# Optimization experiments

Hardware: AMD Instinct MI355X
Metric: run time of the kernel (lower is better)

Reference implementation:

```python
import jax, jax.numpy as jnp
import numpy as np

H = 16          # num_heads
NB = 32         # pos_bias_num_buckets
EPS = 1e-8      # RMSNorm eps


def setup_inputs() -> dict:
    key = jax.random.key(0)
    ks = jax.random.split(key, 8)
    B, L, K, R, M, Dm, Dq = 2, 32, 2, 64, 128, 2048, 2048
    x = jax.random.normal(ks[0], (B, L, K, R, Dm), jnp.float32)
    past_ca_hidden_states = jax.random.normal(ks[1], (B, L, M, Dm), jnp.float32)
    past_ca_attention_mask = jax.random.bernoulli(ks[2], 0.95, (B, L, M)).astype(jnp.float32)
    ln_scale = jnp.ones((Dm,), jnp.float32)
    q_w = jax.random.normal(ks[3], (Dq, Dm), jnp.float32) * 0.02      # torch Linear weight [out,in]
    kv_w = jax.random.normal(ks[4], (2 * Dq, Dm), jnp.float32) * 0.02
    out_w = jax.random.normal(ks[5], (Dm, Dq), jnp.float32) * 0.02
    bias_table = jax.random.normal(ks[6], (NB, H), jnp.float32) * 0.02  # relative_attention_bias.weight
    return dict(x=x, past_ca_hidden_states=past_ca_hidden_states,
                past_ca_attention_mask=past_ca_attention_mask,
                ln_scale=ln_scale, q_w=q_w, kv_w=kv_w, out_w=out_w,
                bias_table=bias_table)


def _rel_bias(bias_table, r, m):
    # linear bucketing, bidirectional=True (RelativePositionBias._relative_position_bucket_linear)
    mn = -(NB // 2) - (NB % 2 - 1)   # -15 for NB=32
    mx = NB // 2                      # 16
    rel = jnp.arange(m)[None, :] - jnp.arange(r)[:, None]   # memory - query, [r, m]
    buckets = jnp.clip(rel, mn, mx) - mn                    # in [0, NB)
    return jnp.transpose(bias_table[buckets], (2, 0, 1))    # [H, r, m]


def reference(x, past_ca_hidden_states, past_ca_attention_mask,
              ln_scale, q_w, kv_w, out_w, bias_table):
    B, L, K, R, Dm = x.shape
    M = past_ca_hidden_states.shape[2]
    Dq = q_w.shape[0]
    dh = Dq // H

    # RMSNorm (p=-1: full norm)
    rms = jnp.linalg.norm(x, axis=-1, keepdims=True) * (Dm ** -0.5)
    xn = (x / (rms + EPS)) * ln_scale

    # projections (no bias)
    q = jnp.einsum('blkrc,qc->blkrq', xn, q_w)                 # [B,L,K,R,Dq]
    kv = jnp.einsum('blmc,qc->blmq', past_ca_hidden_states, kv_w)  # [B,L,M,2Dq]
    k = kv[..., :Dq]
    v = kv[..., Dq:]

    # split heads
    q = q.reshape(B, L, K, R, H, dh).transpose(0, 1, 2, 4, 3, 5)  # [B,L,K,H,R,dh]
    k = k.reshape(B, L, M, H, dh).transpose(0, 1, 3, 2, 4)        # [B,L,H,M,dh]
    v = v.reshape(B, L, M, H, dh).transpose(0, 1, 3, 2, 4)        # [B,L,H,M,dh]

    # NOTE: original applies NO 1/sqrt(dh) scaling
    scores = jnp.einsum('blkhrd,blhmd->blkhrm', q, k)             # [B,L,K,H,R,M]
    scores = scores + _rel_bias(bias_table, R, M)                 # broadcast [H,R,M]
    mask_add = (1.0 - past_ca_attention_mask) * -10000.0          # [B,L,M]
    scores = scores + mask_add[:, :, None, None, None, :]

    attn = jax.nn.softmax(scores, axis=-1)
    out = jnp.einsum('blkhrm,blhmd->blkhrd', attn, v)             # [B,L,K,H,R,dh]
    out = out.transpose(0, 1, 2, 4, 3, 5).reshape(B, L, K, R, Dq)  # merge heads '(h d)'
    out = jnp.einsum('blkrq,cq->blkrc', out, out_w)                # final_proj
    return out + x, attn
```

## Files before the change

### kernel.cpp

```cpp
#include <hip/hip_runtime.h>

typedef _Float16 f16;
typedef _Float16 f16x8 __attribute__((ext_vector_type(8)));
typedef float f32x4 __attribute__((ext_vector_type(4)));

#define LDS_GL16(g, l) __builtin_amdgcn_global_load_lds( \
    (const __attribute__((address_space(1))) void*)(g),  \
    (__attribute__((address_space(3))) void*)(l), 16, 0, 0)
#define VMCNT(N) asm volatile("s_waitcnt vmcnt(" #N ")" ::: "memory")
#define BAR() __builtin_amdgcn_s_barrier()

__global__ __launch_bounds__(256) void conv4_kern(
        const float* __restrict__ s0, f16* __restrict__ d0,
        const float* __restrict__ s1, f16* __restrict__ d1,
        const float* __restrict__ s2, f16* __restrict__ d2,
        const float* __restrict__ s3, f16* __restrict__ d3) {
    int b = blockIdx.x;
    const float* in; f16* out; long base;
    if (b < 2048)       { in = s0; out = d0; base = (long)b * 2048; }
    else if (b < 6144)  { in = s1; out = d1; base = (long)(b - 2048) * 2048; }
    else if (b < 8192)  { in = s2; out = d2; base = (long)(b - 6144) * 2048; }
    else                { in = s3; out = d3; base = (long)(b - 8192) * 2048; }
    long o = base + threadIdx.x * 8;
    float4 a = *(const float4*)(in + o);
    float4 c = *(const float4*)(in + o + 4);
    f16x8 v = { (f16)a.x,(f16)a.y,(f16)a.z,(f16)a.w,
                (f16)c.x,(f16)c.y,(f16)c.z,(f16)c.w };
    *(f16x8*)(out + o) = v;
}

__global__ __launch_bounds__(256) void rmsnorm_kern(const float* __restrict__ x,
                                                    const float* __restrict__ scale,
                                                    f16* __restrict__ out) {
    long base = (long)blockIdx.x * 2048 + threadIdx.x * 8;
    float4 a = *(const float4*)(x + base);
    float4 b = *(const float4*)(x + base + 4);
    float ss = a.x*a.x + a.y*a.y + a.z*a.z + a.w*a.w
             + b.x*b.x + b.y*b.y + b.z*b.z + b.w*b.w;
    #pragma unroll
    for (int d = 1; d < 64; d <<= 1) ss += __shfl_xor(ss, d, 64);
    __shared__ float red[4];
    if ((threadIdx.x & 63) == 0) red[threadIdx.x >> 6] = ss;
    __syncthreads();
    ss = red[0] + red[1] + red[2] + red[3];
    float inv = 1.0f / (sqrtf(ss * (1.0f / 2048.0f)) + 1e-8f);
    int c = threadIdx.x * 8;
    float4 s1 = *(const float4*)(scale + c);
    float4 s2 = *(const float4*)(scale + c + 4);
    f16x8 v = { (f16)(a.x*inv*s1.x),(f16)(a.y*inv*s1.y),(f16)(a.z*inv*s1.z),(f16)(a.w*inv*s1.w),
                (f16)(b.x*inv*s2.x),(f16)(b.y*inv*s2.y),(f16)(b.z*inv*s2.z),(f16)(b.w*inv*s2.w) };
    *(f16x8*)(out + base) = v;
}

template<int EPI>
__device__ __forceinline__ void gemm256_body(
        const f16* __restrict__ A, const f16* __restrict__ B,
        f16* __restrict__ Ch, float* __restrict__ Cf,
        const float* __restrict__ resid, int N, int Kd, int m0, int n0) {
    alignas(16) __shared__ f16 lds[65536];
    int tid = threadIdx.x, lane = tid & 63;
    int wid = tid >> 6, wm = wid >> 2, wn = wid & 3;
    int lr = lane & 15, g = lane >> 4;
    int iL = tid >> 3, cb = tid & 7;

    long goff[8]; int doff[8];
    #pragma unroll
    for (int rd = 0; rd < 2; ++rd) {
        int rA0 = iL + rd * 128;
        goff[0 + rd] = (long)(m0 + rA0) * Kd + ((cb ^ (rA0 & 7)) << 3);
        doff[0 + rd] = rA0 * 64 + cb * 8;
        int rB0 = (iL & 31) + ((iL >> 5) + rd * 2) * 64;
        goff[2 + rd] = (long)(n0 + rB0) * Kd + ((cb ^ (rB0 & 7)) << 3);
        doff[2 + rd] = 32768 + rB0 * 64 + cb * 8;
        int rB1 = rB0 + 32;
        goff[4 + rd] = (long)(n0 + rB1) * Kd + ((cb ^ (rB1 & 7)) << 3);
        doff[4 + rd] = 32768 + rB1 * 64 + cb * 8;
        int rA1 = rA0 + 64;
        goff[6 + rd] = (long)(m0 + rA1) * Kd + ((cb ^ (rA1 & 7)) << 3);
        doff[6 + rd] = rA1 * 64 + cb * 8;
    }
    auto stage = [&](int kt, int p, int r) {
        const f16* src = (r == 0 || r == 3) ? A : B;
        #pragma unroll
        for (int rd = 0; rd < 2; ++rd)
            LDS_GL16(src + goff[r * 2 + rd] + kt * 64,
                     lds + p * 16384 + doff[r * 2 + rd]);
    };

    const char* ldsc = (const char*)lds;
    int swz = lr & 7;
    const char* baseA[2], *baseB[2];
    baseA[0] = ldsc + (wm * 128 + lr) * 128 + ((g ^ swz) << 4);
    baseA[1] = ldsc + (wm * 128 + lr) * 128 + (((4 + g) ^ swz) << 4);
    baseB[0] = ldsc + 65536 + (wn * 64 + lr) * 128 + ((g ^ swz) << 4);
    baseB[1] = ldsc + 65536 + (wn * 64 + lr) * 128 + (((4 + g) ^ swz) << 4);

    f32x4 acc[8][4] = {};
    f16x8 a[4][2], b0[2][2], b1[2][2];

    auto loadA = [&](int bufB, int qm) {
        #pragma unroll
        for (int mf = 0; mf < 4; ++mf)
            #pragma unroll
            for (int kk = 0; kk < 2; ++kk)
                a[mf][kk] = *(const f16x8*)(baseA[kk] + bufB + qm * 8192 + mf * 2048);
    };
    auto loadB = [&](f16x8 (&d)[2][2], int bufB, int qn) {
        #pragma unroll
        for (int nf = 0; nf < 2; ++nf)
            #pragma unroll
            for (int kk = 0; kk < 2; ++kk)
                d[nf][kk] = *(const f16x8*)(baseB[kk] + bufB + qn * 4096 + nf * 2048);
    };
    auto mma = [&](f16x8 (&bb)[2][2], int qm, int qn) {
        __builtin_amdgcn_s_setprio(1);
        #pragma unroll
        for (int kk = 0; kk < 2; ++kk)
            #pragma unroll
            for (int mf = 0; mf < 4; ++mf)
                #pragma unroll
                for (int nf = 0; nf < 2; ++nf)
                    acc[qm * 4 + mf][qn * 2 + nf] = __builtin_amdgcn_mfma_f32_16x16x32_f16(
                        a[mf][kk], bb[nf][kk], acc[qm * 4 + mf][qn * 2 + nf], 0, 0, 0);
        __builtin_amdgcn_s_setprio(0);
    };

    int NT = Kd >> 6, NI = NT >> 1;

    stage(0, 0, 0); stage(0, 0, 1); stage(0, 0, 2); stage(0, 0, 3);
    stage(1, 1, 0); stage(1, 1, 1); stage(1, 1, 2);
    VMCNT(6); BAR();

    for (int it = 0; it < NI - 1; ++it) {
        int t0 = it * 2;
        loadA(0, 0); loadB(b0, 0, 0);
        stage(t0 + 1, 1, 3);
        BAR(); mma(b0, 0, 0); BAR();
        loadB(b1, 0, 1);
        stage(t0 + 2, 0, 0);
        BAR(); mma(b1, 0, 1); BAR();
        loadA(0, 1);
        stage(t0 + 2, 0, 1);
        BAR(); mma(b1, 1, 1); BAR();
        stage(t0 + 2, 0, 2);
        VMCNT(6);
        BAR(); mma(b0, 1, 0); BAR();
        loadA(32768, 0); loadB(b0, 32768, 0);
        stage(t0 + 2, 0, 3);
        BAR(); mma(b0, 0, 0); BAR();
        loadB(b1, 32768, 1);
        stage(t0 + 3, 1, 0);
        BAR(); mma(b1, 0, 1); BAR();
        loadA(32768, 1);
        stage(t0 + 3, 1, 1);
        BAR(); mma(b1, 1, 1); BAR();
        stage(t0 + 3, 1, 2);
        VMCNT(6);
        BAR(); mma(b0, 1, 0); BAR();
    }
    {
        loadA(0, 0); loadB(b0, 0, 0);
        stage(NT - 1, 1, 3);
        BAR(); mma(b0, 0, 0); BAR();
        loadB(b1, 0, 1);
        BAR(); mma(b1, 0, 1); BAR();
        loadA(0, 1);
        BAR(); mma(b1, 1, 1); BAR();
        VMCNT(0);
        BAR(); mma(b0, 1, 0); BAR();
        loadA(32768, 0); loadB(b0, 32768, 0);
        BAR(); mma(b0, 0, 0); BAR();
        loadB(b1, 32768, 1);
        BAR(); mma(b1, 0, 1); BAR();
        loadA(32768, 1);
        BAR(); mma(b1, 1, 1); BAR();
        BAR(); mma(b0, 1, 0);
    }

    __syncthreads();
    if (EPI == 0) {
        #pragma unroll
        for (int i = 0; i < 8; ++i)
            #pragma unroll
            for (int j = 0; j < 4; ++j)
                #pragma unroll
                for (int reg = 0; reg < 4; ++reg)
                    lds[(wm * 128 + i * 16 + g * 4 + reg) * 256 + wn * 64 + j * 16 + lr] =
                        (f16)acc[i][j][reg];
        __syncthreads();
        #pragma unroll
        for (int k = 0; k < 16; ++k) {
            int e = k * 4096 + tid * 8;
            int row = e >> 8, col = e & 255;
            *(f16x8*)(Ch + (long)(m0 + row) * N + n0 + col) = *(const f16x8*)(lds + e);
        }
    } else {
        float* Ct = (float*)lds;
        #pragma unroll
        for (int h = 0; h < 2; ++h) {
            if (h) __syncthreads();
            if (wm == h) {
                #pragma unroll
                for (int i = 0; i < 8; ++i)
                    #pragma unroll
                    for (int j = 0; j < 4; ++j)
                        #pragma unroll
                        for (int reg = 0; reg < 4; ++reg)
                            Ct[(i * 16 + g * 4 + reg) * 256 + wn * 64 + j * 16 + lr] =
                                acc[i][j][reg];
            }
            __syncthreads();
            #pragma unroll
            for (int k = 0; k < 8; ++k) {
                int e = k * 4096 + tid * 8;
                int row = e >> 8, col = e & 255;
                long gi = (long)(m0 + h * 128 + row) * N + n0 + col;
                float4 c0 = *(const float4*)(Ct + e);
                float4 c1 = *(const float4*)(Ct + e + 4);
                float4 r0 = *(const float4*)(resid + gi);
                float4 r1 = *(const float4*)(resid + gi + 4);
                c0.x += r0.x; c0.y += r0.y; c0.z += r0.z; c0.w += r0.w;
                c1.x += r1.x; c1.y += r1.y; c1.z += r1.z; c1.w += r1.w;
                *(float4*)(Cf + gi) = c0;
                *(float4*)(Cf + gi + 4) = c1;
            }
        }
    }
}

__global__ __launch_bounds__(512, 2) void gemm_qkv(
        const f16* __restrict__ Aq, const f16* __restrict__ Bq, f16* __restrict__ Cq,
        const f16* __restrict__ Akv, const f16* __restrict__ Bkv, f16* __restrict__ Ckv) {
    int fid = (blockIdx.x & 7) * 96 + (blockIdx.x >> 3);
    const f16 *A, *B; f16* C; int N, lf, sh;
    if (fid < 256) { A = Aq;  B = Bq;  C = Cq;  N = 2048; lf = fid;       sh = 3; }
    else           { A = Akv; B = Bkv; C = Ckv; N = 4096; lf = fid - 256; sh = 4; }
    int by = lf >> sh, bx = lf & ((1 << sh) - 1);
    gemm256_body<0>(A, B, C, nullptr, nullptr, N, 2048, by << 8, bx << 8);
}

__global__ __launch_bounds__(512, 2) void gemm_out(
        const f16* __restrict__ A, const f16* __restrict__ B,
        float* __restrict__ Cf, const float* __restrict__ resid) {
    int fid = (blockIdx.x & 7) * 32 + (blockIdx.x >> 3);
    int by = fid >> 3, bx = fid & 7;
    gemm256_body<1>(A, B, nullptr, Cf, resid, 2048, 2048, by << 8, bx << 8);
}

__global__ __launch_bounds__(256, 2) void attn_kern(
        const f16* __restrict__ Q,
        const f16* __restrict__ KV,
        const float* __restrict__ mask,
        const float* __restrict__ bias,
        float* __restrict__ attn_out,
        f16* __restrict__ pv_out) {
    __shared__ f16 Vs[128 * 128];
    __shared__ f16 P[64 * 136];
    int blk = blockIdx.x;
    int h  = blk & 15;
    int bk = blk >> 4;
    int bl = bk >> 1;
    int tid = threadIdx.x, lane = tid & 63, w = tid >> 6;
    int r0 = w << 4;
    int lr = lane & 15, g = lane >> 4;
    long qbase  = (long)bk * 64 * 2048;
    long kvbase = (long)bl * 128 * 4096;
    const f16* vsrc = KV + kvbase + 2048 + h * 128;
    {
        int idx = tid;
        #pragma unroll
        for (int rnd = 0; rnd < 8; ++rnd) {
            int vrow = idx >> 4, c = idx & 15;
            LDS_GL16(vsrc + (long)vrow * 4096 + c * 8, Vs + idx * 8);
            idx += 256;
        }
    }
    f16x8 aq[4];
    const f16* qrow = Q + qbase + (long)(r0 + lr) * 2048 + h * 128 + g * 8;
    #pragma unroll
    for (int t4 = 0; t4 < 4; ++t4) aq[t4] = *(const f16x8*)(qrow + t4 * 32);
    f32x4 s[8] = {};
    const f16* kbase = KV + kvbase + h * 128 + g * 8;
    #pragma unroll
    for (int j = 0; j < 8; ++j) {
        #pragma unroll
        for (int t4 = 0; t4 < 4; ++t4) {
            f16x8 bkf = *(const f16x8*)(kbase + (long)(j * 16 + lr) * 4096 + t4 * 32);
            s[j] = __builtin_amdgcn_mfma_f32_16x16x32_f16(aq[t4], bkf, s[j], 0, 0, 0);
        }
    }
    float madd[8];
    #pragma unroll
    for (int j = 0; j < 8; ++j)
        madd[j] = (1.0f - mask[(long)bl * 128 + j * 16 + lr]) * -10000.0f;
    #pragma unroll
    for (int reg = 0; reg < 4; ++reg) {
        int r = r0 + g * 4 + reg;
        float mx = -3.0e38f;
        #pragma unroll
        for (int j = 0; j < 8; ++j) {
            int m = j * 16 + lr;
            int rel = m - r;
            int bkt = (rel < -15 ? -15 : (rel > 16 ? 16 : rel)) + 15;
            float v = s[j][reg] + bias[bkt * 16 + h] + madd[j];
            s[j][reg] = v;
            mx = fmaxf(mx, v);
        }
        #pragma unroll
        for (int d = 1; d < 16; d <<= 1) mx = fmaxf(mx, __shfl_xor(mx, d, 64));
        float sum = 0.0f;
        #pragma unroll
        for (int j = 0; j < 8; ++j) {
            float e = __expf(s[j][reg] - mx);
            s[j][reg] = e;
            sum += e;
        }
        #pragma unroll
        for (int d = 1; d < 16; d <<= 1) sum += __shfl_xor(sum, d, 64);
        float inv = 1.0f / sum;
        #pragma unroll
        for (int j = 0; j < 8; ++j) s[j][reg] *= inv;
    }
    long abase = (long)blk * 64 * 128;
    #pragma unroll
    for (int reg = 0; reg < 4; ++reg) {
        int r = r0 + g * 4 + reg;
        #pragma unroll
        for (int j = 0; j < 8; ++j) {
            attn_out[abase + (long)r * 128 + j * 16 + lr] = s[j][reg];
            P[r * 136 + j * 16 + lr] = (f16)s[j][reg];
        }
    }
    __syncthreads();
    f16x8 pa[4];
    #pragma unroll
    for (int t4 = 0; t4 < 4; ++t4)
        pa[t4] = *(const f16x8*)(P + (r0 + lr) * 136 + t4 * 32 + g * 8);
    f32x4 o[8] = {};
    #pragma unroll
    for (int dj = 0; dj < 8; ++dj) {
        #pragma unroll
        for (int t4 = 0; t4 < 4; ++t4) {
            f16x8 bv;
            #pragma unroll
            for (int rg = 0; rg < 8; ++rg)
                bv[rg] = Vs[(t4 * 32 + g * 8 + rg) * 128 + dj * 16 + lr];
            o[dj] = __builtin_amdgcn_mfma_f32_16x16x32_f16(pa[t4], bv, o[dj], 0, 0, 0);
        }
    }
    __syncthreads();
    #pragma unroll
    for (int dj = 0; dj < 8; ++dj)
        #pragma unroll
        for (int reg = 0; reg < 4; ++reg)
            Vs[(r0 + g * 4 + reg) * 128 + dj * 16 + lr] = (f16)o[dj][reg];
    __syncthreads();
    f16* ob = pv_out + qbase + h * 128;
    #pragma unroll
    for (int k = 0; k < 4; ++k) {
        int e = k * 2048 + tid * 8;
        int row = e >> 7, col = e & 127;
        *(f16x8*)(ob + (long)row * 2048 + col) = *(const f16x8*)(Vs + e);
    }
}

extern "C" void kernel_launch(void* const* d_in, const int* in_sizes, int n_in,
                              void* d_out, int out_size, void* d_ws, size_t ws_size,
                              hipStream_t stream) {
    const float* x     = (const float*)d_in[0];
    const float* hid   = (const float*)d_in[1];
    const float* mask  = (const float*)d_in[2];
    const float* lnsc  = (const float*)d_in[3];
    const float* q_w   = (const float*)d_in[4];
    const float* kv_w  = (const float*)d_in[5];
    const float* out_w = (const float*)d_in[6];
    const float* bias  = (const float*)d_in[7];
    float* out0 = (float*)d_out;
    float* attn = out0 + 16777216;

    f16* kv_h  = (f16*)out0;
    f16* xn_h  = (f16*)attn;
    f16* hid_h = (f16*)(attn + 8388608);
    char* ws = (char*)d_ws;
    f16* q_h    = (f16*)(ws);
    f16* ao_h   = (f16*)(ws + 33554432L);
    f16* qw_h   = (f16*)(ws + 67108864L);
    f16* kvw_h  = (f16*)(ws + 75497472L);
    f16* outw_h = (f16*)(ws + 92274688L);

    conv4_kern<<<16384, 256, 0, stream>>>(q_w, qw_h, kv_w, kvw_h,
                                          out_w, outw_h, hid, hid_h);
    rmsnorm_kern<<<8192, 256, 0, stream>>>(x, lnsc, xn_h);
    gemm_qkv<<<768, 512, 0, stream>>>(xn_h, qw_h, q_h, hid_h, kvw_h, kv_h);
    attn_kern<<<2048, 256, 0, stream>>>(q_h, kv_h, mask, bias, attn, ao_h);
    gemm_out<<<256, 512, 0, stream>>>(ao_h, outw_h, out0, x);
}
```

Baseline: 375.9 us.

## Merge prep kernels, swizzle LDS epilogues, transpose V in LDS for vector loads

Folds the fp16 conversion and RMSNorm launches into one prep kernel, saving a launch. XOR-swizzles the LDS staging in both GEMM epilogues and the attention output to reduce bank conflicts. In attention, V is loaded into registers and written transposed and swizzled into LDS, so the PV MFMA operand becomes one 16-byte LDS read instead of eight scalar reads. This replaces the async global-to-LDS load with register staging and a scalar-store transpose, which adds register pressure and LDS write traffic.

Measured after the change: 370.1 us. No clear change (-1.5%).

```diff
diff --git a/kernel.cpp b/kernel.cpp
--- a/kernel.cpp
+++ b/kernel.cpp
@@ -10,46 +10,46 @@
 #define VMCNT(N) asm volatile("s_waitcnt vmcnt(" #N ")" ::: "memory")
 #define BAR() __builtin_amdgcn_s_barrier()
 
-__global__ __launch_bounds__(256) void conv4_kern(
-        const float* __restrict__ s0, f16* __restrict__ d0,
-        const float* __restrict__ s1, f16* __restrict__ d1,
-        const float* __restrict__ s2, f16* __restrict__ d2,
-        const float* __restrict__ s3, f16* __restrict__ d3) {
+__global__ __launch_bounds__(256) void prep_kern(
+        const float* __restrict__ qw,   f16* __restrict__ qwh,
+        const float* __restrict__ kvw,  f16* __restrict__ kvwh,
+        const float* __restrict__ outw, f16* __restrict__ outwh,
+        const float* __restrict__ hid,  f16* __restrict__ hidh,
+        const float* __restrict__ x, const float* __restrict__ lnsc,
+        f16* __restrict__ xnh) {
     int b = blockIdx.x;
+    if (b >= 16384) {
+        long base = (long)(b - 16384) * 2048 + threadIdx.x * 8;
+        float4 a = *(const float4*)(x + base);
+        float4 v = *(const float4*)(x + base + 4);
+        float ss = a.x*a.x + a.y*a.y + a.z*a.z + a.w*a.w
+                 + v.x*v.x + v.y*v.y + v.z*v.z + v.w*v.w;
+        #pragma unroll
+        for (int d = 1; d < 64; d <<= 1) ss += __shfl_xor(ss, d, 64);
+        __shared__ float red[4];
+        if ((threadIdx.x & 63) == 0) red[threadIdx.x >> 6] = ss;
+        __syncthreads();
+        ss = red[0] + red[1] + red[2] + red[3];
+        float inv = 1.0f / (sqrtf(ss * (1.0f / 2048.0f)) + 1e-8f);
+        int c = threadIdx.x * 8;
+        float4 s1 = *(const float4*)(lnsc + c);
+        float4 s2 = *(const float4*)(lnsc + c + 4);
+        f16x8 o = { (f16)(a.x*inv*s1.x),(f16)(a.y*inv*s1.y),(f16)(a.z*inv*s1.z),(f16)(a.w*inv*s1.w),
+                    (f16)(v.x*inv*s2.x),(f16)(v.y*inv*s2.y),(f16)(v.z*inv*s2.z),(f16)(v.w*inv*s2.w) };
+        *(f16x8*)(xnh + base) = o;
+        return;
+    }
     const float* in; f16* out; long base;
-    if (b < 2048)       { in = s0; out = d0; base = (long)b * 2048; }
-    else if (b < 6144)  { in = s1; out = d1; base = (long)(b - 2048) * 2048; }
-    else if (b < 8192)  { in = s2; out = d2; base = (long)(b - 6144) * 2048; }
-    else                { in = s3; out = d3; base = (long)(b - 8192) * 2048; }
+    if (b < 2048)       { in = qw;   out = qwh;   base = (long)b * 2048; }
+    else if (b < 6144)  { in = kvw;  out = kvwh;  base = (long)(b - 2048) * 2048; }
+    else if (b < 8192)  { in = outw; out = outwh; base = (long)(b - 6144) * 2048; }
+    else                { in = hid;  out = hidh;  base = (long)(b - 8192) * 2048; }
     long o = base + threadIdx.x * 8;
     float4 a = *(const float4*)(in + o);
     float4 c = *(const float4*)(in + o + 4);
     f16x8 v = { (f16)a.x,(f16)a.y,(f16)a.z,(f16)a.w,
                 (f16)c.x,(f16)c.y,(f16)c.z,(f16)c.w };
     *(f16x8*)(out + o) = v;
-}
-
-__global__ __launch_bounds__(256) void rmsnorm_kern(const float* __restrict__ x,
-                                                    const float* __restrict__ scale,
-                                                    f16* __restrict__ out) {
-    long base = (long)blockIdx.x * 2048 + threadIdx.x * 8;
-    float4 a = *(const float4*)(x + base);
-    float4 b = *(const float4*)(x + base + 4);
-    float ss = a.x*a.x + a.y*a.y + a.z*a.z + a.w*a.w
-             + b.x*b.x + b.y*b.y + b.z*b.z + b.w*b.w;
-    #pragma unroll
-    for (int d = 1; d < 64; d <<= 1) ss += __shfl_xor(ss, d, 64);
-    __shared__ float red[4];
-    if ((threadIdx.x & 63) == 0) red[threadIdx.x >> 6] = ss;
-    __syncthreads();
-    ss = red[0] + red[1] + red[2] + red[3];
-    float inv = 1.0f / (sqrtf(ss * (1.0f / 2048.0f)) + 1e-8f);
-    int c = threadIdx.x * 8;
-    float4 s1 = *(const float4*)(scale + c);
-    float4 s2 = *(const float4*)(scale + c + 4);
-    f16x8 v = { (f16)(a.x*inv*s1.x),(f16)(a.y*inv*s1.y),(f16)(a.z*inv*s1.z),(f16)(a.w*inv*s1.w),
-                (f16)(b.x*inv*s2.x),(f16)(b.y*inv*s2.y),(f16)(b.z*inv*s2.z),(f16)(b.w*inv*s2.w) };
-    *(f16x8*)(out + base) = v;
 }
 
 template<int EPI>
@@ -184,15 +184,18 @@
             #pragma unroll
             for (int j = 0; j < 4; ++j)
                 #pragma unroll
-                for (int reg = 0; reg < 4; ++reg)
-                    lds[(wm * 128 + i * 16 + g * 4 + reg) * 256 + wn * 64 + j * 16 + lr] =
-                        (f16)acc[i][j][reg];
+                for (int reg = 0; reg < 4; ++reg) {
+                    int row = wm * 128 + i * 16 + g * 4 + reg;
+                    int col = (wn * 64 + j * 16 + lr) ^ ((row & 12) << 2);
+                    lds[row * 256 + col] = (f16)acc[i][j][reg];
+                }
         __syncthreads();
         #pragma unroll
         for (int k = 0; k < 16; ++k) {
             int e = k * 4096 + tid * 8;
             int row = e >> 8, col = e & 255;
-            *(f16x8*)(Ch + (long)(m0 + row) * N + n0 + col) = *(const f16x8*)(lds + e);
+            *(f16x8*)(Ch + (long)(m0 + row) * N + n0 + col) =
+                *(const f16x8*)(lds + row * 256 + (col ^ ((row & 12) << 2)));
         }
     } else {
         float* Ct = (float*)lds;
@@ -205,18 +208,21 @@
                     #pragma unroll
                     for (int j = 0; j < 4; ++j)
                         #pragma unroll
-                        for (int reg = 0; reg < 4; ++reg)
-                            Ct[(i * 16 + g * 4 + reg) * 256 + wn * 64 + j * 16 + lr] =
-                                acc[i][j][reg];
+                        for (int reg = 0; reg < 4; ++reg) {
+                            int row = i * 16 + g * 4 + reg;
+                            int col = (wn * 64 + j * 16 + lr) ^ ((row & 4) << 2);
+                            Ct[row * 256 + col] = acc[i][j][reg];
+                        }
             }
             __syncthreads();
             #pragma unroll
             for (int k = 0; k < 8; ++k) {
                 int e = k * 4096 + tid * 8;
                 int row = e >> 8, col = e & 255;
+                int pc = col ^ ((row & 4) << 2);
                 long gi = (long)(m0 + h * 128 + row) * N + n0 + col;
-                float4 c0 = *(const float4*)(Ct + e);
-                float4 c1 = *(const float4*)(Ct + e + 4);
+                float4 c0 = *(const float4*)(Ct + row * 256 + pc);
+                float4 c1 = *(const float4*)(Ct + row * 256 + pc + 4);
                 float4 r0 = *(const float4*)(resid + gi);
                 float4 r1 = *(const float4*)(resid + gi + 4);
                 c0.x += r0.x; c0.y += r0.y; c0.z += r0.z; c0.w += r0.w;
@@ -254,7 +260,7 @@
         const float* __restrict__ bias,
         float* __restrict__ attn_out,
         f16* __restrict__ pv_out) {
-    __shared__ f16 Vs[128 * 128];
+    __shared__ f16 Vt[128 * 128];
     __shared__ f16 P[64 * 136];
     int blk = blockIdx.x;
     int h  = blk & 15;
@@ -265,15 +271,12 @@
     int lr = lane & 15, g = lane >> 4;
     long qbase  = (long)bk * 64 * 2048;
     long kvbase = (long)bl * 128 * 4096;
+    f16x8 vreg[8];
     const f16* vsrc = KV + kvbase + 2048 + h * 128;
-    {
-        int idx = tid;
-        #pragma unroll
-        for (int rnd = 0; rnd < 8; ++rnd) {
-            int vrow = idx >> 4, c = idx & 15;
-            LDS_GL16(vsrc + (long)vrow * 4096 + c * 8, Vs + idx * 8);
-            idx += 256;
-        }
+    #pragma unroll
+    for (int rnd = 0; rnd < 8; ++rnd) {
+        int idx = tid + rnd * 256;
+        vreg[rnd] = *(const f16x8*)(vsrc + (long)(idx >> 4) * 4096 + (idx & 15) * 8);
     }
     f16x8 aq[4];
     const f16* qrow = Q + qbase + (long)(r0 + lr) * 2048 + h * 128 + g * 8;
@@ -331,20 +334,35 @@
             P[r * 136 + j * 16 + lr] = (f16)s[j][reg];
         }
     }
+    {
+        char* vtb = (char*)Vt;
+        #pragma unroll
+        for (int rnd = 0; rnd < 8; ++rnd) {
+            int idx = tid + rnd * 256;
+            int k = idx >> 4, c0 = (idx & 15) * 8;
+            #pragma unroll
+            for (int i = 0; i < 8; ++i) {
+                int c = c0 + i;
+                int sx = ((c >> 3) ^ i) & 7;
+                *(f16*)(vtb + c * 256 + ((k * 2) ^ (sx << 4))) = vreg[rnd][i];
+            }
+        }
+    }
     __syncthreads();
     f16x8 pa[4];
     #pragma unroll
     for (int t4 = 0; t4 < 4; ++t4)
         pa[t4] = *(const f16x8*)(P + (r0 + lr) * 136 + t4 * 32 + g * 8);
     f32x4 o[8] = {};
+    const char* vtb = (const char*)Vt;
     #pragma unroll
     for (int dj = 0; dj < 8; ++dj) {
+        int c = dj * 16 + lr;
+        int sc = (((c >> 3) ^ (c & 7)) & 7) << 4;
+        const char* vrow = vtb + c * 256;
         #pragma unroll
         for (int t4 = 0; t4 < 4; ++t4) {
-            f16x8 bv;
-            #pragma unroll
-            for (int rg = 0; rg < 8; ++rg)
-                bv[rg] = Vs[(t4 * 32 + g * 8 + rg) * 128 + dj * 16 + lr];
+            f16x8 bv = *(const f16x8*)(vrow + ((t4 * 64 + g * 16) ^ sc));
             o[dj] = __builtin_amdgcn_mfma_f32_16x16x32_f16(pa[t4], bv, o[dj], 0, 0, 0);
         }
     }
@@ -352,15 +370,19 @@
     #pragma unroll
     for (int dj = 0; dj < 8; ++dj)
         #pragma unroll
-        for (int reg = 0; reg < 4; ++reg)
-            Vs[(r0 + g * 4 + reg) * 128 + dj * 16 + lr] = (f16)o[dj][reg];
+        for (int reg = 0; reg < 4; ++reg) {
+            int row = r0 + g * 4 + reg;
+            int col = (dj * 16 + lr) ^ ((row & 12) << 2);
+            Vt[row * 128 + col] = (f16)o[dj][reg];
+        }
     __syncthreads();
     f16* ob = pv_out + qbase + h * 128;
     #pragma unroll
     for (int k = 0; k < 4; ++k) {
         int e = k * 2048 + tid * 8;
         int row = e >> 7, col = e & 127;
-        *(f16x8*)(ob + (long)row * 2048 + col) = *(const f16x8*)(Vs + e);
+        *(f16x8*)(ob + (long)row * 2048 + col) =
+            *(const f16x8*)(Vt + row * 128 + (col ^ ((row & 12) << 2)));
     }
 }
 
@@ -388,9 +410,9 @@
     f16* kvw_h  = (f16*)(ws + 75497472L);
     f16* outw_h = (f16*)(ws + 92274688L);
 
-    conv4_kern<<<16384, 256, 0, stream>>>(q_w, qw_h, kv_w, kvw_h,
-                                          out_w, outw_h, hid, hid_h);
-    rmsnorm_kern<<<8192, 256, 0, stream>>>(x, lnsc, xn_h);
+    prep_kern<<<24576, 256, 0, stream>>>(q_w, qw_h, kv_w, kvw_h,
+                                         out_w, outw_h, hid, hid_h,
+                                         x, lnsc, xn_h);
     gemm_qkv<<<768, 512, 0, stream>>>(xn_h, qw_h, q_h, hid_h, kvw_h, kv_h);
     attn_kern<<<2048, 256, 0, stream>>>(q_h, kv_h, mask, bias, attn, ao_h);
     gemm_out<<<256, 512, 0, stream>>>(ao_h, outw_h, out0, x);
```
